# Kernel tuning notes

Hardware: AMD Instinct MI355X
Metric: run time of the kernel (lower is better)

Reference implementation:

```python
import jax, jax.numpy as jnp
import numpy as np

N, Wt, Tt, DIM = 16, 256, 2048, 256
EPS = 1e-5

def silu(x):
    return x * jax.nn.sigmoid(x)

def setup_inputs() -> dict:
    key = jax.random.key(0)
    ks = jax.random.split(key, 12)
    d = {}
    d['T'] = jnp.arange(Tt, dtype=jnp.float32)
    d['durations'] = jax.random.uniform(ks[0], (N, Wt, 1), jnp.float32)
    d['features'] = jax.random.normal(ks[1], (N, Wt, DIM), jnp.float32)
    d['conv1_w'] = jax.random.normal(ks[2], (8, DIM, 3), jnp.float32) * 0.05
    d['conv1_b'] = jnp.zeros((8,), jnp.float32)
    d['bn1_g'] = jnp.ones((8,), jnp.float32)
    d['bn1_b'] = jnp.zeros((8,), jnp.float32)
    d['bn1_m'] = jnp.zeros((8,), jnp.float32)
    d['bn1_v'] = jnp.ones((8,), jnp.float32)
    d['conv2_w'] = jax.random.normal(ks[3], (8, DIM, 3), jnp.float32) * 0.05
    d['conv2_b'] = jnp.zeros((8,), jnp.float32)
    d['bn2_g'] = jnp.ones((8,), jnp.float32)
    d['bn2_b'] = jnp.zeros((8,), jnp.float32)
    d['bn2_m'] = jnp.zeros((8,), jnp.float32)
    d['bn2_v'] = jnp.ones((8,), jnp.float32)
    d['sb1_w1'] = jax.random.normal(ks[4], (10, 2), jnp.float32) * 0.3
    d['sb1_b1'] = jnp.zeros((2,), jnp.float32)
    d['sb1_w2'] = jax.random.normal(ks[5], (2, 2), jnp.float32) * 0.3
    d['sb1_b2'] = jnp.zeros((2,), jnp.float32)
    d['sb2_w1'] = jax.random.normal(ks[6], (10, 16), jnp.float32) * 0.3
    d['sb2_b1'] = jnp.zeros((16,), jnp.float32)
    d['sb2_w2'] = jax.random.normal(ks[7], (16, 16), jnp.float32) * 0.3
    d['sb2_b2'] = jnp.zeros((16,), jnp.float32)
    d['proj1_w'] = jax.random.normal(ks[8], (2, DIM), jnp.float32) * 0.3
    d['proj1_b'] = jnp.zeros((DIM,), jnp.float32)
    d['proj2_w'] = jax.random.normal(ks[9], (16, 1), jnp.float32) * 0.3
    d['proj2_b'] = jnp.zeros((1,), jnp.float32)
    return d

def _conv_bn_silu(x_ncw, w, b, g, beta, m, v):
    # Conv1d(dim->8, k=3, pad=1) + BatchNorm(eval) + SiLU
    y = jax.lax.conv_general_dilated(x_ncw, w, (1,), [(1, 1)],
                                     dimension_numbers=('NCH', 'OIH', 'NCH'))
    y = y + b[None, :, None]
    y = (y - m[None, :, None]) * jax.lax.rsqrt(v[None, :, None] + EPS)
    y = y * g[None, :, None] + beta[None, :, None]
    return silu(y)

def _swish_block(x, w1, b1, w2, b2):
    x = silu(x @ w1 + b1)
    return silu(x @ w2 + b2)

def reference(T, durations, features, conv1_w, conv1_b, bn1_g, bn1_b, bn1_m, bn1_v,
              conv2_w, conv2_b, bn2_g, bn2_b, bn2_m, bn2_v,
              sb1_w1, sb1_b1, sb1_w2, sb1_b2, sb2_w1, sb2_b1, sb2_w2, sb2_b2,
              proj1_w, proj1_b, proj2_w, proj2_b):
    feat = jnp.swapaxes(features, 1, 2)  # (N, C, W)
    n, _, w = feat.shape
    t = T.shape[0]
    left = jnp.swapaxes(_conv_bn_silu(feat, conv1_w, conv1_b, bn1_g, bn1_b, bn1_m, bn1_v), 1, 2)   # (N, W, 8)
    right = jnp.swapaxes(_conv_bn_silu(feat, conv2_w, conv2_b, bn2_g, bn2_b, bn2_m, bn2_v), 1, 2)  # (N, W, 8)
    token_end = jnp.cumsum(durations, axis=1)        # (N, W, 1)
    token_start = token_end - durations              # (N, W, 1)
    S = T[None, None, :] - token_start               # (N, W, T)
    E = token_end - T[None, None, :]                 # (N, W, T)
    left_b = jnp.broadcast_to(left[:, :, None, :], (n, w, t, 8))
    right_b = jnp.broadcast_to(right[:, :, None, :], (n, w, t, 8))
    xleft = jnp.concatenate([S[..., None], E[..., None], left_b], axis=-1)    # (N, W, T, 10)
    xright = jnp.concatenate([S[..., None], E[..., None], right_b], axis=-1)  # (N, W, T, 10)
    C = _swish_block(xleft, sb1_w1, sb1_b1, sb1_w2, sb1_b2)                   # (N, W, T, 2)
    xr = _swish_block(xright, sb2_w1, sb2_b1, sb2_w2, sb2_b2)                 # (N, W, T, 16)
    score = (xr @ proj2_w + proj2_b)[..., 0]                                  # (N, W, T)
    Wsm = jax.nn.softmax(score, axis=1)  # softmax over tokens W
    out_r = jnp.einsum('nkt,ndk->ntd', Wsm, feat)                             # (N, T, dim)
    out_l = jnp.einsum('nkt,nktp->ntp', Wsm, C) @ proj1_w + proj1_b           # (N, T, dim)
    return out_l + out_r
```

## Files before the change

kernel.cpp:

```cpp
#include <hip/hip_runtime.h>
#include <hip/hip_bf16.h>

#define NN  16
#define WT  256
#define TT  2048
#define DIM 256
#define TBT 8

typedef __attribute__((ext_vector_type(8))) short short8_t;
typedef __attribute__((ext_vector_type(4))) float f32x4;

__device__ __forceinline__ float fast_rcp(float x){ return __builtin_amdgcn_rcpf(x); }

__device__ __forceinline__ float silu_f(float x){
    return x * fast_rcp(1.0f + __expf(-x));
}

__device__ __forceinline__ unsigned short f2bf(float x){
    union { float f; unsigned u; } v; v.f = x;
    unsigned r = v.u + 0x7FFFu + ((v.u >> 16) & 1u);
    return (unsigned short)(r >> 16);
}

__device__ __forceinline__ void fma4(float4& a, float s, const float4& f){
    a.x = fmaf(s, f.x, a.x); a.y = fmaf(s, f.y, a.y);
    a.z = fmaf(s, f.z, a.z); a.w = fmaf(s, f.w, a.w);
}

__global__ __launch_bounds__(256) void prep_k(
    const float* __restrict__ dur, const float* __restrict__ feat,
    const float* __restrict__ c1w, const float* __restrict__ c1b,
    const float* __restrict__ g1,  const float* __restrict__ be1,
    const float* __restrict__ m1,  const float* __restrict__ vv1,
    const float* __restrict__ c2w, const float* __restrict__ c2b,
    const float* __restrict__ g2,  const float* __restrict__ be2,
    const float* __restrict__ m2,  const float* __restrict__ vv2,
    const float* __restrict__ sb1w1, const float* __restrict__ sb1b1,
    const float* __restrict__ sb2w1, const float* __restrict__ sb2b1,
    float* __restrict__ v1o, float* __restrict__ v2o)
{
    int w = blockIdx.x, n = blockIdx.y;
    int tid = threadIdx.x;

    __shared__ float sdur[WT];
    sdur[tid] = dur[n*WT + tid];
    __syncthreads();
    for (int off = 1; off < WT; off <<= 1){
        float v = (tid >= off) ? sdur[tid-off] : 0.0f;
        __syncthreads();
        sdur[tid] += v;
        __syncthreads();
    }
    float end   = sdur[w];
    float start = end - dur[n*WT + w];

    const float* fb = feat + (size_t)(n*WT)*DIM;
    float fm = (w > 0)    ? fb[(size_t)(w-1)*DIM + tid] : 0.0f;
    float f0 =              fb[(size_t) w   *DIM + tid];
    float fp = (w < WT-1) ? fb[(size_t)(w+1)*DIM + tid] : 0.0f;

    float pl[8], pr[8];
    #pragma unroll
    for (int o = 0; o < 8; o++){
        const float* wp = c1w + (size_t)(o*DIM + tid)*3;
        pl[o] = fmaf(fm, wp[0], fmaf(f0, wp[1], fp*wp[2]));
        const float* wq = c2w + (size_t)(o*DIM + tid)*3;
        pr[o] = fmaf(fm, wq[0], fmaf(f0, wq[1], fp*wq[2]));
    }
    #pragma unroll
    for (int o = 0; o < 8; o++){
        #pragma unroll
        for (int off = 32; off; off >>= 1){
            pl[o] += __shfl_xor(pl[o], off);
            pr[o] += __shfl_xor(pr[o], off);
        }
    }
    __shared__ float sws[4][16];
    int wave = tid >> 6, lane = tid & 63;
    if (lane == 0){
        #pragma unroll
        for (int o = 0; o < 8; o++){ sws[wave][o] = pl[o]; sws[wave][8+o] = pr[o]; }
    }
    __syncthreads();
    __shared__ float slr[16];
    if (tid < 16){
        float s = sws[0][tid] + sws[1][tid] + sws[2][tid] + sws[3][tid];
        int o = tid & 7; bool isr = tid >= 8;
        float bias = isr ? c2b[o] : c1b[o];
        float mm   = isr ? m2[o]  : m1[o];
        float vv   = isr ? vv2[o] : vv1[o];
        float gg   = isr ? g2[o]  : g1[o];
        float bb   = isr ? be2[o] : be1[o];
        float y = s + bias;
        y = (y - mm) * rsqrtf(vv + 1e-5f);
        y = y * gg + bb;
        slr[tid] = silu_f(y);
    }
    __syncthreads();
    if (tid < 16){
        int j = tid;
        float acc = sb2b1[j] - start*sb2w1[j] + end*sb2w1[16 + j];
        #pragma unroll
        for (int o = 0; o < 8; o++) acc = fmaf(slr[8+o], sb2w1[(2+o)*16 + j], acc);
        v2o[(size_t)(n*WT + w)*16 + j] = acc;
    } else if (tid < 18){
        int p = tid - 16;
        float acc = sb1b1[p] - start*sb1w1[p] + end*sb1w1[2 + p];
        #pragma unroll
        for (int o = 0; o < 8; o++) acc = fmaf(slr[o], sb1w1[(2+o)*2 + p], acc);
        v1o[(size_t)(n*WT + w)*2 + p] = acc;
    }
}

__global__ __launch_bounds__(256) void featpack_k(const float* __restrict__ feat,
                                                  unsigned short* __restrict__ featP)
{
    int kb = blockIdx.x, n = blockIdx.y;
    int d = threadIdx.x;
    const float* fb = feat + (size_t)n*WT*DIM + (size_t)kb*32*DIM + d;
    unsigned short* op = featP + ((size_t)(n*8 + kb)*DIM + d)*32;
    unsigned short buf[32];
    #pragma unroll
    for (int e = 0; e < 32; e++) buf[e] = f2bf(fb[(size_t)e*DIM]);
    #pragma unroll
    for (int g = 0; g < 4; g++){
        uint4 u;
        u.x = (unsigned)buf[g*8+0] | ((unsigned)buf[g*8+1] << 16);
        u.y = (unsigned)buf[g*8+2] | ((unsigned)buf[g*8+3] << 16);
        u.z = (unsigned)buf[g*8+4] | ((unsigned)buf[g*8+5] << 16);
        u.w = (unsigned)buf[g*8+6] | ((unsigned)buf[g*8+7] << 16);
        *(uint4*)(op + g*8) = u;
    }
}

__global__ __launch_bounds__(256) void score_k(
    const float* __restrict__ Tg,
    const float* __restrict__ v1g, const float* __restrict__ v2g,
    const float* __restrict__ sb1w1, const float* __restrict__ sb1w2, const float* __restrict__ sb1b2,
    const float* __restrict__ sb2w1, const float* __restrict__ sb2w2, const float* __restrict__ sb2b2,
    const float* __restrict__ p2w, const float* __restrict__ p2b,
    unsigned short* __restrict__ wsm_b, float* __restrict__ wc_g)
{
    int n   = blockIdx.y;
    int t0  = blockIdx.x * TBT;
    int tid = threadIdx.x;
    int w   = tid;
    int lane = tid & 63, wave = tid >> 6;

    __shared__ float s_w2[16*16];
    __shared__ float s_u2[16], s_b2[16], s_p2w[16];
    __shared__ float s_u1[2], s_w21[4], s_b21[2];
    __shared__ float s_xa[4][TBT];
    __shared__ float s_xs[4][TBT];
    __shared__ float s_xc0[4][TBT], s_xc1[4][TBT];

    s_w2[tid] = sb2w2[tid];
    if (tid < 16){
        s_u2[tid]  = sb2w1[tid] - sb2w1[16 + tid];
        s_b2[tid]  = sb2b2[tid];
        s_p2w[tid] = p2w[tid];
    } else if (tid < 18){
        int p = tid - 16;
        s_u1[p]  = sb1w1[p] - sb1w1[2 + p];
        s_b21[p] = sb1b2[p];
    } else if (tid < 22){
        s_w21[tid - 18] = sb1w2[tid - 18];
    }
    __syncthreads();

    float v2r[16];
    {
        const float4* vp = (const float4*)(v2g + (size_t)(n*WT + w)*16);
        float4 a = vp[0], b = vp[1], c = vp[2], d = vp[3];
        v2r[0]=a.x; v2r[1]=a.y; v2r[2]=a.z; v2r[3]=a.w;
        v2r[4]=b.x; v2r[5]=b.y; v2r[6]=b.z; v2r[7]=b.w;
        v2r[8]=c.x; v2r[9]=c.y; v2r[10]=c.z; v2r[11]=c.w;
        v2r[12]=d.x; v2r[13]=d.y; v2r[14]=d.z; v2r[15]=d.w;
    }
    float v1r0, v1r1;
    {
        const float* vp = v1g + (size_t)(n*WT + w)*2;
        v1r0 = vp[0]; v1r1 = vp[1];
    }
    float p2bv = p2b[0];
    float tv[TBT];
    #pragma unroll
    for (int ti = 0; ti < TBT; ti++) tv[ti] = Tg[t0 + ti];

    unsigned mpos = 0u, mneg = 0u;
    #pragma unroll
    for (int i = 0; i < 16; i++){
        float u = s_u2[i], v = v2r[i];
        float xa = fmaf(tv[0],     u, v);
        float xb = fmaf(tv[TBT-1], u, v);
        float lo = fminf(xa, xb), hi = fmaxf(xa, xb);
        if (__all(lo >  20.0f)) mpos |= (1u << i);
        else if (__all(hi < -20.0f)) mneg |= (1u << i);
    }
    unsigned mact = 0xFFFFu & ~(mpos | mneg);

    float scores[TBT];
    if (mact == 0u){
        float hA[16], hB[16];
        #pragma unroll
        for (int j = 0; j < 16; j++){ hA[j] = s_b2[j]; hB[j] = 0.0f; }
        #pragma unroll
        for (int i = 0; i < 16; i++){
            if (mpos & (1u << i)){
                float u = s_u2[i], v = v2r[i];
                #pragma unroll
                for (int j = 0; j < 16; j++){
                    float wv = s_w2[i*16 + j];
                    hA[j] = fmaf(v, wv, hA[j]);
                    hB[j] = fmaf(u, wv, hB[j]);
                }
            }
        }
        unsigned jpos = 0u, jact = 0u;
        #pragma unroll
        for (int j = 0; j < 16; j++){
            float h0 = fmaf(tv[0],     hB[j], hA[j]);
            float h7 = fmaf(tv[TBT-1], hB[j], hA[j]);
            float lo = fminf(h0, h7), hi = fmaxf(h0, h7);
            unsigned p  = (unsigned)__all(lo > 20.0f);
            unsigned nn = (unsigned)__all(hi < -20.0f);
            jpos |= p << j;
            jact |= ((p | nn) ^ 1u) << j;
        }
        float SA = p2bv, SB = 0.0f;
        #pragma unroll
        for (int j = 0; j < 16; j++){
            float pw = s_p2w[j] * (float)((jpos >> j) & 1u);
            SA = fmaf(hA[j], pw, SA);
            SB = fmaf(hB[j], pw, SB);
        }
        #pragma unroll
        for (int ti = 0; ti < TBT; ti++) scores[ti] = fmaf(tv[ti], SB, SA);
        #pragma unroll
        for (int j = 0; j < 16; j++){
            if (jact & (1u << j)){
                float pw = s_p2w[j];
                float a = hA[j], b = hB[j];
                #pragma unroll
                for (int ti = 0; ti < TBT; ti++)
                    scores[ti] = fmaf(silu_f(fmaf(tv[ti], b, a)), pw, scores[ti]);
            }
        }
    } else {
        #pragma unroll
        for (int tp = 0; tp < TBT; tp += 2){
            float h2a[16], h2b[16];
            #pragma unroll
            for (int j = 0; j < 16; j++){ float b = s_b2[j]; h2a[j] = b; h2b[j] = b; }
            #pragma unroll
            for (int i = 0; i < 16; i++){
                if (mneg & (1u << i)) continue;
                float u = s_u2[i], v = v2r[i];
                float aa = fmaf(tv[tp],   u, v);
                float ab = fmaf(tv[tp+1], u, v);
                if (!(mpos & (1u << i))){
                    aa = silu_f(aa);
                    ab = silu_f(ab);
                }
                #pragma unroll
                for (int j = 0; j < 16; j++){
                    float wv = s_w2[i*16 + j];
                    h2a[j] = fmaf(aa, wv, h2a[j]);
                    h2b[j] = fmaf(ab, wv, h2b[j]);
                }
            }
            float sa = p2bv, sb = p2bv;
            #pragma unroll
            for (int j = 0; j < 16; j++){
                float pw = s_p2w[j];
                float ha = h2a[j], hb = h2b[j];
                if (__all(fminf(ha, hb) > 20.0f)){
                    sa = fmaf(ha, pw, sa);
                    sb = fmaf(hb, pw, sb);
                } else if (__all(fmaxf(ha, hb) < -20.0f)){
                } else {
                    sa = fmaf(silu_f(ha), pw, sa);
                    sb = fmaf(silu_f(hb), pw, sb);
                }
            }
            scores[tp] = sa; scores[tp+1] = sb;
        }
    }

    float c0r[TBT], c1r[TBT];
    {
        float u10 = s_u1[0], u11 = s_u1[1];
        float w00 = s_w21[0], w01 = s_w21[1], w10 = s_w21[2], w11 = s_w21[3];
        float b0 = s_b21[0], b1 = s_b21[1];
        float x0a = fmaf(tv[0], u10, v1r0), x0b = fmaf(tv[TBT-1], u10, v1r0);
        float x1a = fmaf(tv[0], u11, v1r1), x1b = fmaf(tv[TBT-1], u11, v1r1);
        bool p0 = __all(fminf(x0a, x0b) >  20.0f);
        bool n0 = __all(fmaxf(x0a, x0b) < -20.0f);
        bool p1 = __all(fminf(x1a, x1b) >  20.0f);
        bool n1 = __all(fmaxf(x1a, x1b) < -20.0f);
        #pragma unroll
        for (int ti = 0; ti < TBT; ti++){
            float x0 = fmaf(tv[ti], u10, v1r0);
            float x1 = fmaf(tv[ti], u11, v1r1);
            float gl0, gl1;
            if (p0)      gl0 = x0;
            else if (n0) gl0 = 0.0f;
            else         gl0 = silu_f(x0);
            if (p1)      gl1 = x1;
            else if (n1) gl1 = 0.0f;
            else         gl1 = silu_f(x1);
            float y0 = fmaf(gl0, w00, fmaf(gl1, w10, b0));
            float y1 = fmaf(gl0, w01, fmaf(gl1, w11, b1));
            if (__all(fminf(y0, y1) > 20.0f)){
                c0r[ti] = y0; c1r[ti] = y1;
            } else if (__all(fmaxf(y0, y1) < -20.0f)){
                c0r[ti] = 0.0f; c1r[ti] = 0.0f;
            } else {
                c0r[ti] = silu_f(y0); c1r[ti] = silu_f(y1);
            }
        }
    }

    float m[TBT];
    #pragma unroll
    for (int ti = 0; ti < TBT; ti++) m[ti] = scores[ti];
    #pragma unroll
    for (int off = 32; off; off >>= 1){
        #pragma unroll
        for (int ti = 0; ti < TBT; ti++) m[ti] = fmaxf(m[ti], __shfl_xor(m[ti], off));
    }
    if (lane == 0){
        #pragma unroll
        for (int ti = 0; ti < TBT; ti++) s_xa[wave][ti] = m[ti];
    }
    __syncthreads();
    #pragma unroll
    for (int ti = 0; ti < TBT; ti++)
        m[ti] = fmaxf(fmaxf(s_xa[0][ti], s_xa[1][ti]), fmaxf(s_xa[2][ti], s_xa[3][ti]));

    float e[TBT], ps[TBT], pc0[TBT], pc1[TBT];
    #pragma unroll
    for (int ti = 0; ti < TBT; ti++){
        e[ti]   = __expf(scores[ti] - m[ti]);
        ps[ti]  = e[ti];
        pc0[ti] = e[ti] * c0r[ti];
        pc1[ti] = e[ti] * c1r[ti];
    }
    #pragma unroll
    for (int off = 32; off; off >>= 1){
        #pragma unroll
        for (int ti = 0; ti < TBT; ti++){
            ps[ti]  += __shfl_xor(ps[ti],  off);
            pc0[ti] += __shfl_xor(pc0[ti], off);
            pc1[ti] += __shfl_xor(pc1[ti], off);
        }
    }
    if (lane == 0){
        #pragma unroll
        for (int ti = 0; ti < TBT; ti++){
            s_xs[wave][ti]  = ps[ti];
            s_xc0[wave][ti] = pc0[ti];
            s_xc1[wave][ti] = pc1[ti];
        }
    }
    __syncthreads();

    unsigned short* wbase = wsm_b + ((size_t)n*TT + t0)*WT + w;
    #pragma unroll
    for (int ti = 0; ti < TBT; ti++){
        float S  = s_xs[0][ti] + s_xs[1][ti] + s_xs[2][ti] + s_xs[3][ti];
        float rS = fast_rcp(S);
        wbase[(size_t)ti*WT] = f2bf(e[ti] * rS);
    }
    if (tid < TBT){
        int ti = tid;
        float S  = s_xs[0][ti] + s_xs[1][ti] + s_xs[2][ti] + s_xs[3][ti];
        float rS = fast_rcp(S);
        float2 wc;
        wc.x = (s_xc0[0][ti] + s_xc0[1][ti] + s_xc0[2][ti] + s_xc0[3][ti]) * rS;
        wc.y = (s_xc1[0][ti] + s_xc1[1][ti] + s_xc1[2][ti] + s_xc1[3][ti]) * rS;
        *(float2*)(wc_g + ((size_t)n*TT + t0 + ti)*2) = wc;
    }
}

__global__ __launch_bounds__(512) void outr_mfma_k(
    const unsigned short* __restrict__ wsmB, const unsigned short* __restrict__ featP,
    const float* __restrict__ wc_g,
    const float* __restrict__ p1w, const float* __restrict__ p1b,
    float* __restrict__ out)
{
    int n    = blockIdx.y;
    int t0   = blockIdx.x * 32;
    int tid  = threadIdx.x;
    int lane = tid & 63, wave = tid >> 6;
    int tw   = t0 + (wave >> 2) * 16;
    int dbase = (wave & 3) * 4;
    int l15  = lane & 15, quad = lane >> 4;

    f32x4 acc[4];
    #pragma unroll
    for (int dt = 0; dt < 4; dt++) acc[dt] = (f32x4){0.f, 0.f, 0.f, 0.f};

    const unsigned short* aPtr = wsmB + ((size_t)(n*TT + tw + l15))*WT + quad*8;

    #pragma unroll
    for (int kb = 0; kb < 8; kb++){
        short8_t af = *(const short8_t*)(aPtr + kb*32);
        const unsigned short* bp = featP + ((size_t)(n*8 + kb)*DIM + dbase*16 + l15)*32 + quad*8;
        #pragma unroll
        for (int dt = 0; dt < 4; dt++){
            short8_t bf = *(const short8_t*)(bp + (size_t)dt*16*32);
            acc[dt] = __builtin_amdgcn_mfma_f32_16x16x32_bf16(af, bf, acc[dt], 0, 0, 0);
        }
    }

    float wc0[4], wc1[4];
    #pragma unroll
    for (int r = 0; r < 4; r++){
        const float* wp = wc_g + ((size_t)(n*TT + tw + quad*4 + r))*2;
        wc0[r] = wp[0]; wc1[r] = wp[1];
    }
    float* obase = out + ((size_t)(n*TT + tw + quad*4))*DIM;
    #pragma unroll
    for (int dt = 0; dt < 4; dt++){
        int d = (dbase + dt)*16 + l15;
        float pa = p1w[d], pb2 = p1w[DIM + d], pc = p1b[d];
        #pragma unroll
        for (int r = 0; r < 4; r++){
            float val = acc[dt][r] + fmaf(wc0[r], pa, fmaf(wc1[r], pb2, pc));
            obase[(size_t)r*DIM + d] = val;
        }
    }
}

__global__ __launch_bounds__(256) void fused_k(
    const float* __restrict__ Tg, const float* __restrict__ feat,
    const float* __restrict__ v1g, const float* __restrict__ v2g,
    const float* __restrict__ sb1w1, const float* __restrict__ sb1w2, const float* __restrict__ sb1b2,
    const float* __restrict__ sb2w1, const float* __restrict__ sb2w2, const float* __restrict__ sb2b2,
    const float* __restrict__ p1w, const float* __restrict__ p1b,
    const float* __restrict__ p2w, const float* __restrict__ p2b,
    float* __restrict__ out)
{
    int n   = blockIdx.y;
    int t0  = blockIdx.x * TBT;
    int tid = threadIdx.x;
    int w   = tid;
    int lane = tid & 63, wave = tid >> 6;

    __shared__ float s_w2[16*16];
    __shared__ float s_u2[16], s_b2[16], s_p2w[16];
    __shared__ float s_u1[2], s_w21[4], s_b21[2];
    __shared__ float s_wsmT[WT][TBT];
    __shared__ float s_xa[4][TBT];
    __shared__ float s_xs[4][TBT];
    __shared__ float s_xc0[4][TBT], s_xc1[4][TBT];
    __shared__ float s_wc0[TBT], s_wc1[TBT];
    __shared__ float s_out[4][DIM];

    s_w2[tid] = sb2w2[tid];
    if (tid < 16){
        s_u2[tid]  = sb2w1[tid] - sb2w1[16 + tid];
        s_b2[tid]  = sb2b2[tid];
        s_p2w[tid] = p2w[tid];
    } else if (tid < 18){
        int p = tid - 16;
        s_u1[p]  = sb1w1[p] - sb1w1[2 + p];
        s_b21[p] = sb1b2[p];
    } else if (tid < 22){
        s_w21[tid - 18] = sb1w2[tid - 18];
    }
    __syncthreads();

    float v2r[16];
    {
        const float4* vp = (const float4*)(v2g + (size_t)(n*WT + w)*16);
        float4 a = vp[0], b = vp[1], c = vp[2], d = vp[3];
        v2r[0]=a.x; v2r[1]=a.y; v2r[2]=a.z; v2r[3]=a.w;
        v2r[4]=b.x; v2r[5]=b.y; v2r[6]=b.z; v2r[7]=b.w;
        v2r[8]=c.x; v2r[9]=c.y; v2r[10]=c.z; v2r[11]=c.w;
        v2r[12]=d.x; v2r[13]=d.y; v2r[14]=d.z; v2r[15]=d.w;
    }
    float v1r0, v1r1;
    {
        const float* vp = v1g + (size_t)(n*WT + w)*2;
        v1r0 = vp[0]; v1r1 = vp[1];
    }
    float p2bv = p2b[0];
    float tv[TBT];
    #pragma unroll
    for (int ti = 0; ti < TBT; ti++) tv[ti] = Tg[t0 + ti];

    float scores[TBT];
    #pragma unroll
    for (int tp = 0; tp < TBT; tp += 2){
        float h2a[16], h2b[16];
        #pragma unroll
        for (int j = 0; j < 16; j++){ float b = s_b2[j]; h2a[j] = b; h2b[j] = b; }
        #pragma unroll
        for (int i = 0; i < 16; i++){
            float u = s_u2[i], v = v2r[i];
            float aa = silu_f(fmaf(tv[tp],   u, v));
            float ab = silu_f(fmaf(tv[tp+1], u, v));
            #pragma unroll
            for (int j = 0; j < 16; j++){
                float wv = s_w2[i*16 + j];
                h2a[j] = fmaf(aa, wv, h2a[j]);
                h2b[j] = fmaf(ab, wv, h2b[j]);
            }
        }
        float sa = p2bv, sb = p2bv;
        #pragma unroll
        for (int j = 0; j < 16; j++){
            float pw = s_p2w[j];
            sa = fmaf(silu_f(h2a[j]), pw, sa);
            sb = fmaf(silu_f(h2b[j]), pw, sb);
        }
        scores[tp] = sa; scores[tp+1] = sb;
    }

    float c0r[TBT], c1r[TBT];
    {
        float u10 = s_u1[0], u11 = s_u1[1];
        float w00 = s_w21[0], w01 = s_w21[1], w10 = s_w21[2], w11 = s_w21[3];
        float b0 = s_b21[0], b1 = s_b21[1];
        #pragma unroll
        for (int ti = 0; ti < TBT; ti++){
            float gl0 = silu_f(fmaf(tv[ti], u10, v1r0));
            float gl1 = silu_f(fmaf(tv[ti], u11, v1r1));
            c0r[ti] = silu_f(fmaf(gl0, w00, fmaf(gl1, w10, b0)));
            c1r[ti] = silu_f(fmaf(gl0, w01, fmaf(gl1, w11, b1)));
        }
    }

    float m[TBT];
    #pragma unroll
    for (int ti = 0; ti < TBT; ti++) m[ti] = scores[ti];
    #pragma unroll
    for (int off = 32; off; off >>= 1){
        #pragma unroll
        for (int ti = 0; ti < TBT; ti++) m[ti] = fmaxf(m[ti], __shfl_xor(m[ti], off));
    }
    if (lane == 0){
        #pragma unroll
        for (int ti = 0; ti < TBT; ti++) s_xa[wave][ti] = m[ti];
    }
    __syncthreads();
    #pragma unroll
    for (int ti = 0; ti < TBT; ti++)
        m[ti] = fmaxf(fmaxf(s_xa[0][ti], s_xa[1][ti]), fmaxf(s_xa[2][ti], s_xa[3][ti]));

    float e[TBT], ps[TBT], pc0[TBT], pc1[TBT];
    #pragma unroll
    for (int ti = 0; ti < TBT; ti++){
        e[ti]  = __expf(scores[ti] - m[ti]);
        ps[ti] = e[ti];
        pc0[ti] = e[ti] * c0r[ti];
        pc1[ti] = e[ti] * c1r[ti];
    }
    #pragma unroll
    for (int off = 32; off; off >>= 1){
        #pragma unroll
        for (int ti = 0; ti < TBT; ti++){
            ps[ti]  += __shfl_xor(ps[ti],  off);
            pc0[ti] += __shfl_xor(pc0[ti], off);
            pc1[ti] += __shfl_xor(pc1[ti], off);
        }
    }
    if (lane == 0){
        #pragma unroll
        for (int ti = 0; ti < TBT; ti++){
            s_xs[wave][ti]  = ps[ti];
            s_xc0[wave][ti] = pc0[ti];
            s_xc1[wave][ti] = pc1[ti];
        }
    }
    __syncthreads();
    #pragma unroll
    for (int ti = 0; ti < TBT; ti++){
        float S  = s_xs[0][ti] + s_xs[1][ti] + s_xs[2][ti] + s_xs[3][ti];
        float rS = fast_rcp(S);
        s_wsmT[w][ti] = e[ti] * rS;
    }
    if (tid < TBT){
        int ti = tid;
        float S  = s_xs[0][ti] + s_xs[1][ti] + s_xs[2][ti] + s_xs[3][ti];
        float rS = fast_rcp(S);
        s_wc0[ti] = (s_xc0[0][ti] + s_xc0[1][ti] + s_xc0[2][ti] + s_xc0[3][ti]) * rS;
        s_wc1[ti] = (s_xc1[0][ti] + s_xc1[1][ti] + s_xc1[2][ti] + s_xc1[3][ti]) * rS;
    }
    __syncthreads();

    int wid = wave;
    int dq  = lane;
    const float* fbase = feat + (size_t)n*WT*DIM + dq*4;
    float4 acc[TBT];
    #pragma unroll
    for (int i = 0; i < TBT; i++) acc[i] = make_float4(0.f, 0.f, 0.f, 0.f);

    #pragma unroll 4
    for (int w0 = wid; w0 < WT; w0 += 4){
        float4 f = *(const float4*)(fbase + (size_t)w0*DIM);
        const float4* wp = (const float4*)&s_wsmT[w0][0];
        float4 wA = wp[0], wB = wp[1];
        fma4(acc[0], wA.x, f); fma4(acc[1], wA.y, f);
        fma4(acc[2], wA.z, f); fma4(acc[3], wA.w, f);
        fma4(acc[4], wB.x, f); fma4(acc[5], wB.y, f);
        fma4(acc[6], wB.z, f); fma4(acc[7], wB.w, f);
    }

    float pw0 = p1w[tid], pw1 = p1w[DIM + tid], pbv = p1b[tid];
    float* orow = out + ((size_t)n*TT + t0)*DIM;
    #pragma unroll
    for (int ti = 0; ti < TBT; ti++){
        __syncthreads();
        *(float4*)&s_out[wid][dq*4] = acc[ti];
        __syncthreads();
        float r = s_out[0][tid] + s_out[1][tid] + s_out[2][tid] + s_out[3][tid];
        float o = fmaf(s_wc0[ti], pw0, fmaf(s_wc1[ti], pw1, r + pbv));
        orow[(size_t)ti*DIM + tid] = o;
    }
}

extern "C" void kernel_launch(void* const* d_in, const int* in_sizes, int n_in,
                              void* d_out, int out_size, void* d_ws, size_t ws_size,
                              hipStream_t stream)
{
    const float* Tg    = (const float*)d_in[0];
    const float* dur   = (const float*)d_in[1];
    const float* feat  = (const float*)d_in[2];
    const float* c1w   = (const float*)d_in[3];
    const float* c1b   = (const float*)d_in[4];
    const float* bn1g  = (const float*)d_in[5];
    const float* bn1b  = (const float*)d_in[6];
    const float* bn1m  = (const float*)d_in[7];
    const float* bn1v  = (const float*)d_in[8];
    const float* c2w   = (const float*)d_in[9];
    const float* c2b   = (const float*)d_in[10];
    const float* bn2g  = (const float*)d_in[11];
    const float* bn2b  = (const float*)d_in[12];
    const float* bn2m  = (const float*)d_in[13];
    const float* bn2v  = (const float*)d_in[14];
    const float* sb1w1 = (const float*)d_in[15];
    const float* sb1b1 = (const float*)d_in[16];
    const float* sb1w2 = (const float*)d_in[17];
    const float* sb1b2 = (const float*)d_in[18];
    const float* sb2w1 = (const float*)d_in[19];
    const float* sb2b1 = (const float*)d_in[20];
    const float* sb2w2 = (const float*)d_in[21];
    const float* sb2b2 = (const float*)d_in[22];
    const float* p1w   = (const float*)d_in[23];
    const float* p1b   = (const float*)d_in[24];
    const float* p2w   = (const float*)d_in[25];
    const float* p2b   = (const float*)d_in[26];
    float* out = (float*)d_out;

    float* ws = (float*)d_ws;
    float* v1  = ws;
    float* v2  = ws + 8192;
    float* wc  = ws + 8192 + 65536;
    unsigned short* wsmB  = (unsigned short*)(ws + 8192 + 65536 + 65536);
    unsigned short* featP = wsmB + (size_t)NN*TT*WT;
    size_t need = ((size_t)8192 + 65536 + 65536)*sizeof(float)
                + ((size_t)NN*TT*WT + (size_t)NN*WT*DIM)*sizeof(unsigned short);

    prep_k<<<dim3(WT, NN), 256, 0, stream>>>(dur, feat, c1w, c1b, bn1g, bn1b, bn1m, bn1v,
                                             c2w, c2b, bn2g, bn2b, bn2m, bn2v,
                                             sb1w1, sb1b1, sb2w1, sb2b1, v1, v2);
    if (ws_size >= need){
        featpack_k<<<dim3(8, NN), 256, 0, stream>>>(feat, featP);
        score_k<<<dim3(TT/TBT, NN), 256, 0, stream>>>(Tg, v1, v2,
                                                      sb1w1, sb1w2, sb1b2,
                                                      sb2w1, sb2w2, sb2b2,
                                                      p2w, p2b, wsmB, wc);
        outr_mfma_k<<<dim3(TT/32, NN), 512, 0, stream>>>(wsmB, featP, wc, p1w, p1b, out);
    } else {
        fused_k<<<dim3(TT/TBT, NN), 256, 0, stream>>>(Tg, feat, v1, v2,
                                                      sb1w1, sb1w2, sb1b2,
                                                      sb2w1, sb2w2, sb2b2,
                                                      p1w, p1b, p2w, p2b, out);
    }
}
```

Before: 277.9 us.

## Split score kernel into score-compute and softmax kernels via fp32 scratch

Splits the fused score kernel into two kernels. The first computes the sb2 swish-block scores and writes them to a new fp32 scratch buffer. The second reads them back, computes the sb1 branch, and does the softmax over tokens plus the weighted-C reduction. The aim is to lower register pressure and raise occupancy in each part. In exchange it adds an extra kernel launch and a 32 MB fp32 write and read round trip. The new path only runs when the workspace is large enough.

```diff
diff --git a/kernel.cpp b/kernel.cpp
--- a/kernel.cpp
+++ b/kernel.cpp
@@ -130,6 +130,275 @@
         u.z = (unsigned)buf[g*8+4] | ((unsigned)buf[g*8+5] << 16);
         u.w = (unsigned)buf[g*8+6] | ((unsigned)buf[g*8+7] << 16);
         *(uint4*)(op + g*8) = u;
+    }
+}
+
+__global__ __launch_bounds__(256) void score1_k(
+    const float* __restrict__ Tg, const float* __restrict__ v2g,
+    const float* __restrict__ sb2w1, const float* __restrict__ sb2w2, const float* __restrict__ sb2b2,
+    const float* __restrict__ p2w, const float* __restrict__ p2b,
+    float* __restrict__ scr)
+{
+    int n   = blockIdx.y;
+    int t0  = blockIdx.x * TBT;
+    int tid = threadIdx.x;
+    int w   = tid;
+
+    __shared__ float s_w2[16*16];
+    __shared__ float s_u2[16], s_b2[16], s_p2w[16];
+
+    s_w2[tid] = sb2w2[tid];
+    if (tid < 16){
+        s_u2[tid]  = sb2w1[tid] - sb2w1[16 + tid];
+        s_b2[tid]  = sb2b2[tid];
+        s_p2w[tid] = p2w[tid];
+    }
+    __syncthreads();
+
+    float v2r[16];
+    {
+        const float4* vp = (const float4*)(v2g + (size_t)(n*WT + w)*16);
+        float4 a = vp[0], b = vp[1], c = vp[2], d = vp[3];
+        v2r[0]=a.x; v2r[1]=a.y; v2r[2]=a.z; v2r[3]=a.w;
+        v2r[4]=b.x; v2r[5]=b.y; v2r[6]=b.z; v2r[7]=b.w;
+        v2r[8]=c.x; v2r[9]=c.y; v2r[10]=c.z; v2r[11]=c.w;
+        v2r[12]=d.x; v2r[13]=d.y; v2r[14]=d.z; v2r[15]=d.w;
+    }
+    float p2bv = p2b[0];
+    float tv[TBT];
+    #pragma unroll
+    for (int ti = 0; ti < TBT; ti++) tv[ti] = Tg[t0 + ti];
+
+    unsigned mpos = 0u, mneg = 0u;
+    #pragma unroll
+    for (int i = 0; i < 16; i++){
+        float u = s_u2[i], v = v2r[i];
+        float xa = fmaf(tv[0],     u, v);
+        float xb = fmaf(tv[TBT-1], u, v);
+        float lo = fminf(xa, xb), hi = fmaxf(xa, xb);
+        if (__all(lo >  20.0f)) mpos |= (1u << i);
+        else if (__all(hi < -20.0f)) mneg |= (1u << i);
+    }
+    unsigned mact = 0xFFFFu & ~(mpos | mneg);
+
+    float scores[TBT];
+    if (mact == 0u){
+        float hA[16], hB[16];
+        #pragma unroll
+        for (int j = 0; j < 16; j++){ hA[j] = s_b2[j]; hB[j] = 0.0f; }
+        #pragma unroll
+        for (int i = 0; i < 16; i++){
+            if (mpos & (1u << i)){
+                float u = s_u2[i], v = v2r[i];
+                #pragma unroll
+                for (int j = 0; j < 16; j++){
+                    float wv = s_w2[i*16 + j];
+                    hA[j] = fmaf(v, wv, hA[j]);
+                    hB[j] = fmaf(u, wv, hB[j]);
+                }
+            }
+        }
+        unsigned jpos = 0u, jact = 0u;
+        #pragma unroll
+        for (int j = 0; j < 16; j++){
+            float h0 = fmaf(tv[0],     hB[j], hA[j]);
+            float h7 = fmaf(tv[TBT-1], hB[j], hA[j]);
+            float lo = fminf(h0, h7), hi = fmaxf(h0, h7);
+            unsigned p  = (unsigned)__all(lo > 20.0f);
+            unsigned nn = (unsigned)__all(hi < -20.0f);
+            jpos |= p << j;
+            jact |= ((p | nn) ^ 1u) << j;
+        }
+        float SA = p2bv, SB = 0.0f;
+        #pragma unroll
+        for (int j = 0; j < 16; j++){
+            float pw = s_p2w[j] * (float)((jpos >> j) & 1u);
+            SA = fmaf(hA[j], pw, SA);
+            SB = fmaf(hB[j], pw, SB);
+        }
+        #pragma unroll
+        for (int ti = 0; ti < TBT; ti++) scores[ti] = fmaf(tv[ti], SB, SA);
+        #pragma unroll
+        for (int j = 0; j < 16; j++){
+            if (jact & (1u << j)){
+                float pw = s_p2w[j];
+                float a = hA[j], b = hB[j];
+                #pragma unroll
+                for (int ti = 0; ti < TBT; ti++)
+                    scores[ti] = fmaf(silu_f(fmaf(tv[ti], b, a)), pw, scores[ti]);
+            }
+        }
+    } else {
+        #pragma unroll
+        for (int tp = 0; tp < TBT; tp += 2){
+            float h2a[16], h2b[16];
+            #pragma unroll
+            for (int j = 0; j < 16; j++){ float b = s_b2[j]; h2a[j] = b; h2b[j] = b; }
+            #pragma unroll
+            for (int i = 0; i < 16; i++){
+                if (mneg & (1u << i)) continue;
+                float u = s_u2[i], v = v2r[i];
+                float aa = fmaf(tv[tp],   u, v);
+                float ab = fmaf(tv[tp+1], u, v);
+                if (!(mpos & (1u << i))){
+                    aa = silu_f(aa);
+                    ab = silu_f(ab);
+                }
+                #pragma unroll
+                for (int j = 0; j < 16; j++){
+                    float wv = s_w2[i*16 + j];
+                    h2a[j] = fmaf(aa, wv, h2a[j]);
+                    h2b[j] = fmaf(ab, wv, h2b[j]);
+                }
+            }
+            float sa = p2bv, sb = p2bv;
+            #pragma unroll
+            for (int j = 0; j < 16; j++){
+                float pw = s_p2w[j];
+                float ha = h2a[j], hb = h2b[j];
+                if (__all(fminf(ha, hb) > 20.0f)){
+                    sa = fmaf(ha, pw, sa);
+                    sb = fmaf(hb, pw, sb);
+                } else if (__all(fmaxf(ha, hb) < -20.0f)){
+                } else {
+                    sa = fmaf(silu_f(ha), pw, sa);
+                    sb = fmaf(silu_f(hb), pw, sb);
+                }
+            }
+            scores[tp] = sa; scores[tp+1] = sb;
+        }
+    }
+
+    float* sbase = scr + ((size_t)n*TT + t0)*WT + w;
+    #pragma unroll
+    for (int ti = 0; ti < TBT; ti++) sbase[(size_t)ti*WT] = scores[ti];
+}
+
+__global__ __launch_bounds__(256) void score2_k(
+    const float* __restrict__ Tg, const float* __restrict__ v1g,
+    const float* __restrict__ scr,
+    const float* __restrict__ sb1w1, const float* __restrict__ sb1w2, const float* __restrict__ sb1b2,
+    unsigned short* __restrict__ wsm_b, float* __restrict__ wc_g)
+{
+    int n   = blockIdx.y;
+    int t0  = blockIdx.x * TBT;
+    int tid = threadIdx.x;
+    int w   = tid;
+    int lane = tid & 63, wave = tid >> 6;
+
+    __shared__ float s_xa[4][TBT];
+    __shared__ float s_xs[4][TBT];
+    __shared__ float s_xc0[4][TBT], s_xc1[4][TBT];
+
+    float v1r0, v1r1;
+    {
+        const float* vp = v1g + (size_t)(n*WT + w)*2;
+        v1r0 = vp[0]; v1r1 = vp[1];
+    }
+    float tv[TBT];
+    #pragma unroll
+    for (int ti = 0; ti < TBT; ti++) tv[ti] = Tg[t0 + ti];
+
+    float scores[TBT];
+    {
+        const float* sbase = scr + ((size_t)n*TT + t0)*WT + w;
+        #pragma unroll
+        for (int ti = 0; ti < TBT; ti++) scores[ti] = sbase[(size_t)ti*WT];
+    }
+
+    float c0r[TBT], c1r[TBT];
+    {
+        float u10 = sb1w1[0] - sb1w1[2], u11 = sb1w1[1] - sb1w1[3];
+        float w00 = sb1w2[0], w01 = sb1w2[1], w10 = sb1w2[2], w11 = sb1w2[3];
+        float b0 = sb1b2[0], b1 = sb1b2[1];
+        float x0a = fmaf(tv[0], u10, v1r0), x0b = fmaf(tv[TBT-1], u10, v1r0);
+        float x1a = fmaf(tv[0], u11, v1r1), x1b = fmaf(tv[TBT-1], u11, v1r1);
+        bool p0 = __all(fminf(x0a, x0b) >  20.0f);
+        bool n0 = __all(fmaxf(x0a, x0b) < -20.0f);
+        bool p1 = __all(fminf(x1a, x1b) >  20.0f);
+        bool n1 = __all(fmaxf(x1a, x1b) < -20.0f);
+        #pragma unroll
+        for (int ti = 0; ti < TBT; ti++){
+            float x0 = fmaf(tv[ti], u10, v1r0);
+            float x1 = fmaf(tv[ti], u11, v1r1);
+            float gl0, gl1;
+            if (p0)      gl0 = x0;
+            else if (n0) gl0 = 0.0f;
+            else         gl0 = silu_f(x0);
+            if (p1)      gl1 = x1;
+            else if (n1) gl1 = 0.0f;
+            else         gl1 = silu_f(x1);
+            float y0 = fmaf(gl0, w00, fmaf(gl1, w10, b0));
+            float y1 = fmaf(gl0, w01, fmaf(gl1, w11, b1));
+            if (__all(fminf(y0, y1) > 20.0f)){
+                c0r[ti] = y0; c1r[ti] = y1;
+            } else if (__all(fmaxf(y0, y1) < -20.0f)){
+                c0r[ti] = 0.0f; c1r[ti] = 0.0f;
+            } else {
+                c0r[ti] = silu_f(y0); c1r[ti] = silu_f(y1);
+            }
+        }
+    }
+
+    float m[TBT];
+    #pragma unroll
+    for (int ti = 0; ti < TBT; ti++) m[ti] = scores[ti];
+    #pragma unroll
+    for (int off = 32; off; off >>= 1){
+        #pragma unroll
+        for (int ti = 0; ti < TBT; ti++) m[ti] = fmaxf(m[ti], __shfl_xor(m[ti], off));
+    }
+    if (lane == 0){
+        #pragma unroll
+        for (int ti = 0; ti < TBT; ti++) s_xa[wave][ti] = m[ti];
+    }
+    __syncthreads();
+    #pragma unroll
+    for (int ti = 0; ti < TBT; ti++)
+        m[ti] = fmaxf(fmaxf(s_xa[0][ti], s_xa[1][ti]), fmaxf(s_xa[2][ti], s_xa[3][ti]));
+
+    float e[TBT], ps[TBT], pc0[TBT], pc1[TBT];
+    #pragma unroll
+    for (int ti = 0; ti < TBT; ti++){
+        e[ti]   = __expf(scores[ti] - m[ti]);
+        ps[ti]  = e[ti];
+        pc0[ti] = e[ti] * c0r[ti];
+        pc1[ti] = e[ti] * c1r[ti];
+    }
+    #pragma unroll
+    for (int off = 32; off; off >>= 1){
+        #pragma unroll
+        for (int ti = 0; ti < TBT; ti++){
+            ps[ti]  += __shfl_xor(ps[ti],  off);
+            pc0[ti] += __shfl_xor(pc0[ti], off);
+            pc1[ti] += __shfl_xor(pc1[ti], off);
+        }
+    }
+    if (lane == 0){
+        #pragma unroll
+        for (int ti = 0; ti < TBT; ti++){
+            s_xs[wave][ti]  = ps[ti];
+            s_xc0[wave][ti] = pc0[ti];
+            s_xc1[wave][ti] = pc1[ti];
+        }
+    }
+    __syncthreads();
+
+    unsigned short* wbase = wsm_b + ((size_t)n*TT + t0)*WT + w;
+    #pragma unroll
+    for (int ti = 0; ti < TBT; ti++){
+        float S  = s_xs[0][ti] + s_xs[1][ti] + s_xs[2][ti] + s_xs[3][ti];
+        float rS = fast_rcp(S);
+        wbase[(size_t)ti*WT] = f2bf(e[ti] * rS);
+    }
+    if (tid < TBT){
+        int ti = tid;
+        float S  = s_xs[0][ti] + s_xs[1][ti] + s_xs[2][ti] + s_xs[3][ti];
+        float rS = fast_rcp(S);
+        float2 wc;
+        wc.x = (s_xc0[0][ti] + s_xc0[1][ti] + s_xc0[2][ti] + s_xc0[3][ti]) * rS;
+        wc.y = (s_xc1[0][ti] + s_xc1[1][ti] + s_xc1[2][ti] + s_xc1[3][ti]) * rS;
+        *(float2*)(wc_g + ((size_t)n*TT + t0 + ti)*2) = wc;
     }
 }
 
@@ -661,13 +930,24 @@
     float* wc  = ws + 8192 + 65536;
     unsigned short* wsmB  = (unsigned short*)(ws + 8192 + 65536 + 65536);
     unsigned short* featP = wsmB + (size_t)NN*TT*WT;
-    size_t need = ((size_t)8192 + 65536 + 65536)*sizeof(float)
-                + ((size_t)NN*TT*WT + (size_t)NN*WT*DIM)*sizeof(unsigned short);
+    float* scr = (float*)(featP + (size_t)NN*WT*DIM);
+    size_t need_old = ((size_t)8192 + 65536 + 65536)*sizeof(float)
+                    + ((size_t)NN*TT*WT + (size_t)NN*WT*DIM)*sizeof(unsigned short);
+    size_t need_split = need_old + (size_t)NN*TT*WT*sizeof(float);
 
     prep_k<<<dim3(WT, NN), 256, 0, stream>>>(dur, feat, c1w, c1b, bn1g, bn1b, bn1m, bn1v,
                                              c2w, c2b, bn2g, bn2b, bn2m, bn2v,
                                              sb1w1, sb1b1, sb2w1, sb2b1, v1, v2);
-    if (ws_size >= need){
+    if (ws_size >= need_split){
+        featpack_k<<<dim3(8, NN), 256, 0, stream>>>(feat, featP);
+        score1_k<<<dim3(TT/TBT, NN), 256, 0, stream>>>(Tg, v2,
+                                                       sb2w1, sb2w2, sb2b2,
+                                                       p2w, p2b, scr);
+        score2_k<<<dim3(TT/TBT, NN), 256, 0, stream>>>(Tg, v1, scr,
+                                                       sb1w1, sb1w2, sb1b2,
+                                                       wsmB, wc);
+        outr_mfma_k<<<dim3(TT/32, NN), 512, 0, stream>>>(wsmB, featP, wc, p1w, p1b, out);
+    } else if (ws_size >= need_old){
         featpack_k<<<dim3(8, NN), 256, 0, stream>>>(feat, featP);
         score_k<<<dim3(TT/TBT, NN), 256, 0, stream>>>(Tg, v1, v2,
                                                       sb1w1, sb1w2, sb1b2,
```

Result: no change. 279.8 us (+0.7%).
